# Kernel optimization log

Hardware: AMD Instinct MI355X
Metric: run time of the kernel (lower is better)

Reference implementation:

```python
import jax, jax.numpy as jnp
import numpy as np

N = 100000   # nodes
E = 800000   # edges
F_IN = 64    # num_node_features
H = 64       # hidden_channels
C = 10       # num_classes


def setup_inputs() -> dict:
    key = jax.random.key(0)
    ks = jax.random.split(key, 12)
    def w(k, fan_in, fan_out):
        return (jax.random.normal(k, (fan_in, fan_out), jnp.float32)
                / np.sqrt(fan_in).astype(np.float32))
    x = jax.random.normal(ks[0], (N, F_IN), jnp.float32)
    edge_index = jax.random.randint(ks[1], (2, E), 0, N, dtype=jnp.int32).astype(jnp.int64)
    return {
        "x": x,
        "edge_index": edge_index,
        # GraphConv 1: lin_rel (with bias) on aggregated, lin_root (no bias) on x
        "W1_rel": w(ks[2], F_IN, H), "b1": jnp.zeros((H,), jnp.float32), "W1_root": w(ks[3], F_IN, H),
        # GraphConv 2
        "W2_rel": w(ks[4], H, H), "b2": jnp.zeros((H,), jnp.float32), "W2_root": w(ks[5], H, H),
        # GCNConv 3
        "W3": w(ks[6], H, H), "b3": jnp.zeros((H,), jnp.float32),
        # final Linear head
        "Wlin": w(ks[7], H, C), "blin": jnp.zeros((C,), jnp.float32),
    }


def _graph_conv(x, src, dst, W_rel, b_rel, W_root):
    # PyG GraphConv (aggr='add'): out = W_rel @ sum_{j->i} x_j + b_rel + W_root @ x_i
    agg = jax.ops.segment_sum(x[src], dst, num_segments=N)  # [N, F] scatter-add
    return agg @ W_rel + b_rel + x @ W_root


def _gcn_conv(x, src, dst, W, b):
    # PyG GCNConv: add self-loops, symmetric norm D^-1/2 (A+I) D^-1/2, then X W + b
    xw = x @ W
    loops = jnp.arange(N, dtype=src.dtype)
    src2 = jnp.concatenate([src, loops])
    dst2 = jnp.concatenate([dst, loops])
    deg = jax.ops.segment_sum(jnp.ones_like(dst2, dtype=xw.dtype), dst2, num_segments=N)
    dinv = jax.lax.rsqrt(deg)  # deg >= 1 thanks to self-loops
    norm = dinv[src2] * dinv[dst2]  # [E+N]
    out = jax.ops.segment_sum(xw[src2] * norm[:, None], dst2, num_segments=N)
    return out + b


def reference(x, edge_index, W1_rel, b1, W1_root, W2_rel, b2, W2_root, W3, b3, Wlin, blin):
    src, dst = edge_index[0], edge_index[1]
    h = jax.nn.relu(_graph_conv(x, src, dst, W1_rel, b1, W1_root))
    h = jax.nn.relu(_graph_conv(h, src, dst, W2_rel, b2, W2_root))
    h = _gcn_conv(h, src, dst, W3, b3)
    # task='node_classification' -> no pooling; dropout is identity in eval mode
    return h @ Wlin + blin
```

## Files before the change

### kernel.cpp

```cpp
#include <hip/hip_runtime.h>

#define NN 100000
#define NE 800000
#define BSH 9
#define BSZ (1 << BSH)
#define NBUK ((NN + BSZ - 1) / BSZ)
#define CAP_E 5120
#define CAP_C 7168
#define ECHUNK 4096
#define GRID_C ((NE + ECHUNK - 1) / ECHUNK)

typedef _Float16 half8 __attribute__((ext_vector_type(8)));
typedef float f32x4 __attribute__((ext_vector_type(4)));

__global__ __launch_bounds__(256) void k_bucket(const int* __restrict__ ei,
    int* __restrict__ bucket_cnt, int* __restrict__ ebuf) {
  __shared__ int h[256];
  __shared__ int cur[256];
  const int tid = threadIdx.x;
  h[tid] = 0;
  __syncthreads();

  const int e0 = blockIdx.x * ECHUNK;
  int pk[16], bk[16];
#pragma unroll
  for (int i = 0; i < 16; ++i) {
    int e = e0 + i * 256 + tid;
    if (e < NE) {
      int src = ei[e];
      int dst = ei[NE + e];
      int b = dst >> BSH;
      pk[i] = src | ((dst & (BSZ - 1)) << 17);
      bk[i] = b;
      atomicAdd(&h[b], 1);
    } else bk[i] = -1;
  }
  __syncthreads();
  cur[tid] = (tid < NBUK && h[tid] > 0) ? atomicAdd(&bucket_cnt[tid], h[tid]) : 0;
  __syncthreads();
#pragma unroll
  for (int i = 0; i < 16; ++i) {
    if (bk[i] >= 0) {
      int slot = atomicAdd(&cur[bk[i]], 1);
      ebuf[bk[i] * CAP_E + slot] = pk[i];
    }
  }
}

__global__ __launch_bounds__(256) void k_csr_build(const int* __restrict__ bucket_cnt,
    const int* __restrict__ ebuf, int2* __restrict__ rp2, int* __restrict__ csr,
    float* __restrict__ dinv) {
  __shared__ int h[BSZ];
  __shared__ int loff[BSZ];
  __shared__ int cur[BSZ];
  __shared__ int sd[256];
  const int tid = threadIdx.x;
  const int b = blockIdx.x;
  h[tid] = 0; h[tid + 256] = 0;
  __syncthreads();

  const int n = bucket_cnt[b];
  const int ebase = b * CAP_E;
  for (int i = tid; i < n; i += 256)
    atomicAdd(&h[ebuf[ebase + i] >> 17], 1);
  __syncthreads();

  int r0 = h[2 * tid], r1 = h[2 * tid + 1];
  int p0 = (r0 + 7) & ~7, p1 = (r1 + 7) & ~7;
  int ps = p0 + p1;
  sd[tid] = ps;
  __syncthreads();
  int incl = ps;
  for (int o = 1; o < 256; o <<= 1) {
    int add = (tid >= o) ? sd[tid - o] : 0;
    __syncthreads();
    incl += add;
    sd[tid] = incl;
    __syncthreads();
  }
  int ex = incl - ps;
  loff[2 * tid] = ex;
  loff[2 * tid + 1] = ex + p0;
  cur[2 * tid] = ex;
  cur[2 * tid + 1] = ex + p0;
  __syncthreads();

  const int node0 = b * BSZ;
  const int cbase = b * CAP_C;
#pragma unroll
  for (int t = 0; t < 2; ++t) {
    int j = tid + t * 256;
    int node = node0 + j;
    if (node < NN) {
      int hr = h[j];
      int hp = (hr + 7) & ~7;
      int beg = cbase + loff[j];
      rp2[node] = make_int2(beg, beg + hp);
      dinv[node] = rsqrtf((float)hr + 1.0f);
      for (int p = hr; p < hp; ++p) csr[beg + p] = NN;
    }
  }

  for (int i = tid; i < n; i += 256) {
    int v = ebuf[ebase + i];
    int dl = v >> 17;
    int slot = atomicAdd(&cur[dl], 1);
    csr[cbase + slot] = v & 0x1FFFF;
  }
}

__global__ __launch_bounds__(256) void k_prep(
    const float* __restrict__ W1r, const float* __restrict__ W1o,
    const float* __restrict__ W2r, const float* __restrict__ W2o,
    const float* __restrict__ W3, const float* __restrict__ b3,
    const float* __restrict__ Wlin, const float* __restrict__ blin,
    const float* __restrict__ x,
    _Float16* __restrict__ W12, _Float16* __restrict__ W34h,
    float* __restrict__ cvec, int* __restrict__ bucket_cnt,
    _Float16* __restrict__ xh, _Float16* __restrict__ Ah, _Float16* __restrict__ P)
{
  int m = blockIdx.x, tid = threadIdx.x;
  if (m >= 4) {
    int idx = (m - 4) * 256 + tid;
    const float4* p4 = (const float4*)(x + idx * 8);
    float4 a = p4[0], b = p4[1];
    half8 h;
    h[0] = (_Float16)a.x; h[1] = (_Float16)a.y; h[2] = (_Float16)a.z; h[3] = (_Float16)a.w;
    h[4] = (_Float16)b.x; h[5] = (_Float16)b.y; h[6] = (_Float16)b.z; h[7] = (_Float16)b.w;
    *(half8*)(xh + idx * 8) = h;
    return;
  }
  if (m < 2) {
    const float* Wr = m ? W2r : W1r;
    const float* Wo = m ? W2o : W1o;
    _Float16* dst = W12 + m * 8192;
    for (int idx = tid; idx < 8192; idx += 256) {
      int n = idx >> 7, k = idx & 127;
      float v = (k < 64) ? Wr[k * 64 + n] : Wo[(k - 64) * 64 + n];
      dst[idx] = (_Float16)v;
    }
  } else if (m == 2) {
    for (int idx = tid; idx < 1024; idx += 256) {
      int c = idx >> 6, k = idx & 63;
      float s = 0.f;
      if (c < 10)
        for (int j = 0; j < 64; ++j) s = fmaf(W3[k * 64 + j], Wlin[j * 10 + c], s);
      W34h[idx] = (_Float16)s;
    }
    if (tid < 10) {
      float s = blin[tid];
      for (int j = 0; j < 64; ++j) s = fmaf(b3[j], Wlin[j * 10 + tid], s);
      cvec[tid] = s;
    }
  } else {
    bucket_cnt[tid] = 0;
    if (tid < 64) {
      xh[NN * 64 + tid] = (_Float16)0.f;
      Ah[NN * 64 + tid] = (_Float16)0.f;
    }
    if (tid < 16) P[NN * 16 + tid] = (_Float16)0.f;
  }
}

template<bool PSTAGE>
__global__ __launch_bounds__(512) void k_layer(
    const _Float16* __restrict__ Ain, const int2* __restrict__ rp2,
    const int* __restrict__ csr, const _Float16* __restrict__ W12,
    const float* __restrict__ bias, const float* __restrict__ dinv,
    _Float16* __restrict__ Aout, const _Float16* __restrict__ W34h,
    _Float16* __restrict__ P)
{
  __shared__ _Float16 sW[64 * 128];
  __shared__ _Float16 sA[128 * 128];
  __shared__ _Float16 sW34[PSTAGE ? 16 * 64 : 8];

  const int tid = threadIdx.x;
  const int node0 = blockIdx.x * 128;
  const int l = tid & 63, w = tid >> 6;

  {
    const uint4* g4 = (const uint4*)W12;
#pragma unroll
    for (int i = 0; i < 2; ++i) {
      int c = tid + 512 * i;
      int n = c >> 4, kc = c & 15;
      *(uint4*)((char*)sW + n * 256 + ((kc * 16) ^ ((n & 7) << 4))) = g4[c];
    }
    if (PSTAGE && tid < 128) {
      int n = tid >> 3, kc = tid & 7;
      uint4 v = ((const uint4*)W34h)[tid];
      *(uint4*)((char*)sW34 + n * 128 + ((kc * 16) ^ ((n & 7) << 4))) = v;
    }
  }

  const int grp = l >> 3, c8 = l & 7;
#pragma unroll
  for (int r = 0; r < 2; ++r) {
    int nl = r * 64 + w * 8 + grp;
    int node = node0 + nl;
    float acc[8];
#pragma unroll
    for (int j = 0; j < 8; ++j) acc[j] = 0.f;
    half8 selfv = {};
    if (node < NN) {
      int2 se = rp2[node];
      for (int i = se.x; i < se.y; i += 8) {
        int4 sa = *(const int4*)(csr + i);
        int4 sb = *(const int4*)(csr + i + 4);
        half8 v0 = *(const half8*)(Ain + sa.x * 64 + c8 * 8);
        half8 v1 = *(const half8*)(Ain + sa.y * 64 + c8 * 8);
        half8 v2 = *(const half8*)(Ain + sa.z * 64 + c8 * 8);
        half8 v3 = *(const half8*)(Ain + sa.w * 64 + c8 * 8);
        half8 v4 = *(const half8*)(Ain + sb.x * 64 + c8 * 8);
        half8 v5 = *(const half8*)(Ain + sb.y * 64 + c8 * 8);
        half8 v6 = *(const half8*)(Ain + sb.z * 64 + c8 * 8);
        half8 v7 = *(const half8*)(Ain + sb.w * 64 + c8 * 8);
#pragma unroll
        for (int j = 0; j < 8; ++j)
          acc[j] += (((float)v0[j] + (float)v1[j]) + ((float)v2[j] + (float)v3[j]))
                  + (((float)v4[j] + (float)v5[j]) + ((float)v6[j] + (float)v7[j]));
      }
      selfv = *(const half8*)(Ain + node * 64 + c8 * 8);
    }
    half8 ha;
#pragma unroll
    for (int j = 0; j < 8; ++j) ha[j] = (_Float16)acc[j];
    char* rowp = (char*)sA + nl * 256;
    int swz = (nl & 7) << 4;
    *(half8*)(rowp + ((c8 * 16) ^ swz)) = ha;
    *(half8*)(rowp + ((128 + c8 * 16) ^ swz)) = selfv;
  }
  __syncthreads();

  const int lm = l & 15, lh = l >> 4;
  f32x4 acc[4];
#pragma unroll
  for (int nt = 0; nt < 4; ++nt) acc[nt] = (f32x4){0.f, 0.f, 0.f, 0.f};

  const int arow = w * 16 + lm;
  const int aswz = (arow & 7) << 4;
#pragma unroll
  for (int kb = 0; kb < 4; ++kb) {
    half8 af = *(half8*)((char*)sA + arow * 256 + ((kb * 64 + lh * 16) ^ aswz));
#pragma unroll
    for (int nt = 0; nt < 4; ++nt) {
      int n = nt * 16 + lm;
      half8 bf = *(half8*)((char*)sW + n * 256 + ((kb * 64 + lh * 16) ^ ((n & 7) << 4)));
      acc[nt] = __builtin_amdgcn_mfma_f32_16x16x32_f16(af, bf, acc[nt], 0, 0, 0);
    }
  }

  if (!PSTAGE) {
#pragma unroll
    for (int nt = 0; nt < 4; ++nt) {
      int col = nt * 16 + lm;
      float bv = bias[col];
#pragma unroll
      for (int r2 = 0; r2 < 4; ++r2) {
        int row = node0 + w * 16 + lh * 4 + r2;
        if (row < NN)
          Aout[row * 64 + col] = (_Float16)fmaxf(acc[nt][r2] + bv, 0.f);
      }
    }
  } else {
#pragma unroll
    for (int r2 = 0; r2 < 4; ++r2) {
      int lrow = w * 16 + lh * 4 + r2;
      int grow = node0 + lrow;
      float s = (grow < NN) ? dinv[grow] : 0.f;
      char* rowp = (char*)sA + lrow * 256;
      int swz = (lrow & 7) << 4;
#pragma unroll
      for (int nt = 0; nt < 4; ++nt) {
        int col = nt * 16 + lm;
        float v = fmaxf(acc[nt][r2] + bias[col], 0.f) * s;
        *(_Float16*)(rowp + ((col * 2) ^ swz)) = (_Float16)v;
      }
    }
    f32x4 accP = (f32x4){0.f, 0.f, 0.f, 0.f};
#pragma unroll
    for (int kb = 0; kb < 2; ++kb) {
      half8 af = *(half8*)((char*)sA + arow * 256 + ((kb * 64 + lh * 16) ^ aswz));
      half8 bf = *(half8*)((char*)sW34 + lm * 128 + ((kb * 64 + lh * 16) ^ ((lm & 7) << 4)));
      accP = __builtin_amdgcn_mfma_f32_16x16x32_f16(af, bf, accP, 0, 0, 0);
    }
#pragma unroll
    for (int r2 = 0; r2 < 4; ++r2) {
      int row = node0 + w * 16 + lh * 4 + r2;
      if (row < NN) P[row * 16 + lm] = (_Float16)accP[r2];
    }
  }
}

__global__ __launch_bounds__(256) void k_head2(const int2* __restrict__ rp2,
    const int* __restrict__ csr, const _Float16* __restrict__ P,
    const float* __restrict__ dinv, const float* __restrict__ cvecg,
    float* __restrict__ out)
{
  __shared__ float sc[10];
  const int tid = threadIdx.x;
  if (tid < 10) sc[tid] = cvecg[tid];
  __syncthreads();

  const int node = blockIdx.x * 128 + (tid >> 1);
  const int half = tid & 1;
  if (node >= NN) return;
  int2 se = rp2[node];

  float acc[8];
#pragma unroll
  for (int j = 0; j < 8; ++j) acc[j] = 0.f;

  for (int i = se.x; i < se.y; i += 8) {
    int4 sa = *(const int4*)(csr + i);
    int4 sb = *(const int4*)(csr + i + 4);
    half8 v0 = *(const half8*)(P + sa.x * 16 + half * 8);
    half8 v1 = *(const half8*)(P + sa.y * 16 + half * 8);
    half8 v2 = *(const half8*)(P + sa.z * 16 + half * 8);
    half8 v3 = *(const half8*)(P + sa.w * 16 + half * 8);
    half8 v4 = *(const half8*)(P + sb.x * 16 + half * 8);
    half8 v5 = *(const half8*)(P + sb.y * 16 + half * 8);
    half8 v6 = *(const half8*)(P + sb.z * 16 + half * 8);
    half8 v7 = *(const half8*)(P + sb.w * 16 + half * 8);
#pragma unroll
    for (int j = 0; j < 8; ++j)
      acc[j] += (((float)v0[j] + (float)v1[j]) + ((float)v2[j] + (float)v3[j]))
              + (((float)v4[j] + (float)v5[j]) + ((float)v6[j] + (float)v7[j]));
  }
  half8 selfv = *(const half8*)(P + node * 16 + half * 8);
#pragma unroll
  for (int j = 0; j < 8; ++j) acc[j] += (float)selfv[j];

  float dv = dinv[node];
  if (half == 0) {
#pragma unroll
    for (int j = 0; j < 4; ++j) {
      float2 o;
      o.x = fmaf(dv, acc[2 * j], sc[2 * j]);
      o.y = fmaf(dv, acc[2 * j + 1], sc[2 * j + 1]);
      *(float2*)(out + node * 10 + 2 * j) = o;
    }
  } else {
    float2 o;
    o.x = fmaf(dv, acc[0], sc[8]);
    o.y = fmaf(dv, acc[1], sc[9]);
    *(float2*)(out + node * 10 + 8) = o;
  }
}

extern "C" void kernel_launch(void* const* d_in, const int* in_sizes, int n_in,
                              void* d_out, int out_size, void* d_ws, size_t ws_size,
                              hipStream_t stream) {
  const float* x       = (const float*)d_in[0];
  const int*   ei      = (const int*)d_in[1];
  const float* W1_rel  = (const float*)d_in[2];
  const float* b1      = (const float*)d_in[3];
  const float* W1_root = (const float*)d_in[4];
  const float* W2_rel  = (const float*)d_in[5];
  const float* b2      = (const float*)d_in[6];
  const float* W2_root = (const float*)d_in[7];
  const float* W3      = (const float*)d_in[8];
  const float* b3      = (const float*)d_in[9];
  const float* Wlin    = (const float*)d_in[10];
  const float* blin    = (const float*)d_in[11];
  float* out = (float*)d_out;

  char* ws = (char*)d_ws;
  _Float16* xh   = (_Float16*)(ws);
  _Float16* Ah   = (_Float16*)(ws + 12800128);
  float*    dinv = (float*)(ws + 25600256);
  int2*     rp2  = (int2*) (ws + 26000256);
  int*      csr  = (int*)  (ws + 26800256);
  _Float16* W12  = (_Float16*)(ws + 32419968);
  _Float16* W34h = (_Float16*)(ws + 32452736);
  float*    cvec = (float*)(ws + 32454784);
  int* bucket_cnt= (int*)  (ws + 32454848);
  _Float16* P    = (_Float16*)(ws + 32455872);
  int* ebuf      = (int*)  (ws + 35655904);

  dim3 b256(256), b512(512);

  k_prep<<<3129, b256, 0, stream>>>(W1_rel, W1_root, W2_rel, W2_root, W3, b3, Wlin,
                                    blin, x, W12, W34h, cvec, bucket_cnt, xh, Ah, P);
  k_bucket<<<GRID_C, b256, 0, stream>>>(ei, bucket_cnt, ebuf);
  k_csr_build<<<NBUK, b256, 0, stream>>>(bucket_cnt, ebuf, rp2, csr, dinv);

  const int gl = (NN + 127) / 128;

  k_layer<false><<<gl, b512, 0, stream>>>(xh, rp2, csr, W12, b1, nullptr, Ah,
                                          nullptr, nullptr);
  k_layer<true><<<gl, b512, 0, stream>>>(Ah, rp2, csr, W12 + 8192, b2, dinv, nullptr,
                                         W34h, P);
  k_head2<<<gl, b256, 0, stream>>>(rp2, csr, P, dinv, cvec, out);
}
```

Measured before the change: 106.5 us.

## Bucket edges per chunk without global atomics and fuse bucketing into setup kernel

Edge bucketing now writes into per-(chunk, bucket) slots of fixed capacity, with no global atomic counter, and is folded into the setup kernel as extra blocks. This removes one kernel launch and the global atomics. The CSR build kernel then prefix-scans the per-chunk counts, gathers each bucket's edges into shared memory, and builds the CSR as before. The risk is overflow if any chunk-bucket holds more than 64 edges or any bucket more than 6144 edges, which relies on the uniformly random destinations. The gather step is also serial per chunk thread.

```diff
diff --git a/kernel.cpp b/kernel.cpp
--- a/kernel.cpp
+++ b/kernel.cpp
@@ -5,121 +5,55 @@
 #define BSH 9
 #define BSZ (1 << BSH)
 #define NBUK ((NN + BSZ - 1) / BSZ)
-#define CAP_E 5120
+#define NCHUNK 196
+#define CAPB 64
 #define CAP_C 7168
-#define ECHUNK 4096
-#define GRID_C ((NE + ECHUNK - 1) / ECHUNK)
 
 typedef _Float16 half8 __attribute__((ext_vector_type(8)));
 typedef float f32x4 __attribute__((ext_vector_type(4)));
 
-__global__ __launch_bounds__(256) void k_bucket(const int* __restrict__ ei,
-    int* __restrict__ bucket_cnt, int* __restrict__ ebuf) {
-  __shared__ int h[256];
-  __shared__ int cur[256];
-  const int tid = threadIdx.x;
-  h[tid] = 0;
-  __syncthreads();
-
-  const int e0 = blockIdx.x * ECHUNK;
-  int pk[16], bk[16];
-#pragma unroll
-  for (int i = 0; i < 16; ++i) {
-    int e = e0 + i * 256 + tid;
-    if (e < NE) {
-      int src = ei[e];
-      int dst = ei[NE + e];
-      int b = dst >> BSH;
-      pk[i] = src | ((dst & (BSZ - 1)) << 17);
-      bk[i] = b;
-      atomicAdd(&h[b], 1);
-    } else bk[i] = -1;
-  }
-  __syncthreads();
-  cur[tid] = (tid < NBUK && h[tid] > 0) ? atomicAdd(&bucket_cnt[tid], h[tid]) : 0;
-  __syncthreads();
-#pragma unroll
-  for (int i = 0; i < 16; ++i) {
-    if (bk[i] >= 0) {
-      int slot = atomicAdd(&cur[bk[i]], 1);
-      ebuf[bk[i] * CAP_E + slot] = pk[i];
-    }
-  }
-}
-
-__global__ __launch_bounds__(256) void k_csr_build(const int* __restrict__ bucket_cnt,
-    const int* __restrict__ ebuf, int2* __restrict__ rp2, int* __restrict__ csr,
-    float* __restrict__ dinv) {
-  __shared__ int h[BSZ];
-  __shared__ int loff[BSZ];
-  __shared__ int cur[BSZ];
-  __shared__ int sd[256];
-  const int tid = threadIdx.x;
-  const int b = blockIdx.x;
-  h[tid] = 0; h[tid + 256] = 0;
-  __syncthreads();
-
-  const int n = bucket_cnt[b];
-  const int ebase = b * CAP_E;
-  for (int i = tid; i < n; i += 256)
-    atomicAdd(&h[ebuf[ebase + i] >> 17], 1);
-  __syncthreads();
-
-  int r0 = h[2 * tid], r1 = h[2 * tid + 1];
-  int p0 = (r0 + 7) & ~7, p1 = (r1 + 7) & ~7;
-  int ps = p0 + p1;
-  sd[tid] = ps;
-  __syncthreads();
-  int incl = ps;
-  for (int o = 1; o < 256; o <<= 1) {
-    int add = (tid >= o) ? sd[tid - o] : 0;
-    __syncthreads();
-    incl += add;
-    sd[tid] = incl;
-    __syncthreads();
-  }
-  int ex = incl - ps;
-  loff[2 * tid] = ex;
-  loff[2 * tid + 1] = ex + p0;
-  cur[2 * tid] = ex;
-  cur[2 * tid + 1] = ex + p0;
-  __syncthreads();
-
-  const int node0 = b * BSZ;
-  const int cbase = b * CAP_C;
-#pragma unroll
-  for (int t = 0; t < 2; ++t) {
-    int j = tid + t * 256;
-    int node = node0 + j;
-    if (node < NN) {
-      int hr = h[j];
-      int hp = (hr + 7) & ~7;
-      int beg = cbase + loff[j];
-      rp2[node] = make_int2(beg, beg + hp);
-      dinv[node] = rsqrtf((float)hr + 1.0f);
-      for (int p = hr; p < hp; ++p) csr[beg + p] = NN;
-    }
-  }
-
-  for (int i = tid; i < n; i += 256) {
-    int v = ebuf[ebase + i];
-    int dl = v >> 17;
-    int slot = atomicAdd(&cur[dl], 1);
-    csr[cbase + slot] = v & 0x1FFFF;
-  }
-}
-
-__global__ __launch_bounds__(256) void k_prep(
+__global__ __launch_bounds__(256) void k_setup(
     const float* __restrict__ W1r, const float* __restrict__ W1o,
     const float* __restrict__ W2r, const float* __restrict__ W2o,
     const float* __restrict__ W3, const float* __restrict__ b3,
     const float* __restrict__ Wlin, const float* __restrict__ blin,
-    const float* __restrict__ x,
+    const float* __restrict__ x, const int* __restrict__ ei,
     _Float16* __restrict__ W12, _Float16* __restrict__ W34h,
-    float* __restrict__ cvec, int* __restrict__ bucket_cnt,
-    _Float16* __restrict__ xh, _Float16* __restrict__ Ah, _Float16* __restrict__ P)
+    float* __restrict__ cvec,
+    _Float16* __restrict__ xh, _Float16* __restrict__ Ah, _Float16* __restrict__ P,
+    int* __restrict__ cnt2, int* __restrict__ ebuf2)
 {
-  int m = blockIdx.x, tid = threadIdx.x;
+  const int m = blockIdx.x, tid = threadIdx.x;
+
+  if (m >= 3129) {
+    __shared__ int curs[256];
+    const int c = m - 3129;
+    curs[tid] = 0;
+    __syncthreads();
+    const int e0 = c * 4096;
+    int pk[16], bk[16];
+#pragma unroll
+    for (int i = 0; i < 16; ++i) {
+      int e = e0 + i * 256 + tid;
+      if (e < NE) {
+        int src = ei[e];
+        int dst = ei[NE + e];
+        bk[i] = dst >> BSH;
+        pk[i] = src | ((dst & (BSZ - 1)) << 17);
+      } else bk[i] = -1;
+    }
+#pragma unroll
+    for (int i = 0; i < 16; ++i) {
+      if (bk[i] >= 0) {
+        int slot = atomicAdd(&curs[bk[i]], 1);
+        ebuf2[(c * NBUK + bk[i]) * CAPB + slot] = pk[i];
+      }
+    }
+    __syncthreads();
+    if (tid < NBUK) cnt2[c * NBUK + tid] = curs[tid];
+    return;
+  }
+
   if (m >= 4) {
     int idx = (m - 4) * 256 + tid;
     const float4* p4 = (const float4*)(x + idx * 8);
@@ -130,6 +64,7 @@
     *(half8*)(xh + idx * 8) = h;
     return;
   }
+
   if (m < 2) {
     const float* Wr = m ? W2r : W1r;
     const float* Wo = m ? W2o : W1o;
@@ -153,12 +88,97 @@
       cvec[tid] = s;
     }
   } else {
-    bucket_cnt[tid] = 0;
     if (tid < 64) {
       xh[NN * 64 + tid] = (_Float16)0.f;
       Ah[NN * 64 + tid] = (_Float16)0.f;
     }
     if (tid < 16) P[NN * 16 + tid] = (_Float16)0.f;
+  }
+}
+
+__global__ __launch_bounds__(256) void k_csr2(const int* __restrict__ cnt2,
+    const int* __restrict__ ebuf2, int2* __restrict__ rp2, int* __restrict__ csr,
+    float* __restrict__ dinv)
+{
+  __shared__ int stage[6144];
+  __shared__ int h[BSZ];
+  __shared__ int loff[BSZ];
+  __shared__ int cur[BSZ];
+  __shared__ int sd[256];
+  __shared__ int cbase[NCHUNK];
+  __shared__ int ntot;
+  const int tid = threadIdx.x;
+  const int b = blockIdx.x;
+  h[tid] = 0; h[tid + 256] = 0;
+
+  int v = (tid < NCHUNK) ? cnt2[tid * NBUK + b] : 0;
+  sd[tid] = v;
+  __syncthreads();
+  int incl = v;
+  for (int o = 1; o < 256; o <<= 1) {
+    int add = (tid >= o) ? sd[tid - o] : 0;
+    __syncthreads();
+    incl += add;
+    sd[tid] = incl;
+    __syncthreads();
+  }
+  if (tid < NCHUNK) cbase[tid] = incl - v;
+  if (tid == 255) ntot = incl;
+  __syncthreads();
+
+  if (tid < NCHUNK) {
+    const int* src = ebuf2 + (tid * NBUK + b) * CAPB;
+    int base = cbase[tid];
+    for (int i = 0; i < v; ++i) stage[base + i] = src[i];
+  }
+  __syncthreads();
+  const int n = ntot;
+
+  for (int i = tid; i < n; i += 256)
+    atomicAdd(&h[stage[i] >> 17], 1);
+  __syncthreads();
+
+  int r0 = h[2 * tid], r1 = h[2 * tid + 1];
+  int p0 = (r0 + 7) & ~7, p1 = (r1 + 7) & ~7;
+  int ps = p0 + p1;
+  sd[tid] = ps;
+  __syncthreads();
+  int incl2 = ps;
+  for (int o = 1; o < 256; o <<= 1) {
+    int add = (tid >= o) ? sd[tid - o] : 0;
+    __syncthreads();
+    incl2 += add;
+    sd[tid] = incl2;
+    __syncthreads();
+  }
+  int ex = incl2 - ps;
+  loff[2 * tid] = ex;
+  loff[2 * tid + 1] = ex + p0;
+  cur[2 * tid] = ex;
+  cur[2 * tid + 1] = ex + p0;
+  __syncthreads();
+
+  const int node0 = b * BSZ;
+  const int cbase2 = b * CAP_C;
+#pragma unroll
+  for (int t = 0; t < 2; ++t) {
+    int j = tid + t * 256;
+    int node = node0 + j;
+    if (node < NN) {
+      int hr = h[j];
+      int hp = (hr + 7) & ~7;
+      int beg = cbase2 + loff[j];
+      rp2[node] = make_int2(beg, beg + hp);
+      dinv[node] = rsqrtf((float)hr + 1.0f);
+      for (int p = hr; p < hp; ++p) csr[beg + p] = NN;
+    }
+  }
+
+  for (int i = tid; i < n; i += 256) {
+    int w = stage[i];
+    int dl = w >> 17;
+    int slot = atomicAdd(&cur[dl], 1);
+    csr[cbase2 + slot] = w & 0x1FFFF;
   }
 }
 
@@ -374,16 +394,16 @@
   _Float16* W12  = (_Float16*)(ws + 32419968);
   _Float16* W34h = (_Float16*)(ws + 32452736);
   float*    cvec = (float*)(ws + 32454784);
-  int* bucket_cnt= (int*)  (ws + 32454848);
-  _Float16* P    = (_Float16*)(ws + 32455872);
-  int* ebuf      = (int*)  (ws + 35655904);
+  _Float16* P    = (_Float16*)(ws + 32454848);
+  int*      cnt2 = (int*)  (ws + 35654880);
+  int*      ebuf2= (int*)  (ws + 35808544);
 
   dim3 b256(256), b512(512);
 
-  k_prep<<<3129, b256, 0, stream>>>(W1_rel, W1_root, W2_rel, W2_root, W3, b3, Wlin,
-                                    blin, x, W12, W34h, cvec, bucket_cnt, xh, Ah, P);
-  k_bucket<<<GRID_C, b256, 0, stream>>>(ei, bucket_cnt, ebuf);
-  k_csr_build<<<NBUK, b256, 0, stream>>>(bucket_cnt, ebuf, rp2, csr, dinv);
+  k_setup<<<3325, b256, 0, stream>>>(W1_rel, W1_root, W2_rel, W2_root, W3, b3, Wlin,
+                                     blin, x, ei, W12, W34h, cvec, xh, Ah, P,
+                                     cnt2, ebuf2);
+  k_csr2<<<NBUK, b256, 0, stream>>>(cnt2, ebuf2, rp2, csr, dinv);
 
   const int gl = (NN + 127) / 128;
 
```

After: 96.76 us, median of 2. -9.1%, faster.
